# Optimization experiments

Hardware: AMD Instinct MI355X
Metric: run time of the kernel (lower is better)

The kernel has to match this reference:

```python
import jax, jax.numpy as jnp
import numpy as np

N = 6144      # nodes
IN = 512      # input_dim
D = 256       # HIDDEN_DIM (out_features per head)
H = 1         # HEADS
OUT = 128     # OUT_DIM
ALPHA = 0.2   # LeakyReLU slope
EPS = 1e-5    # LayerNorm eps


def _xavier(k, shape):
    fan_in, fan_out = shape[-2], shape[-1]
    lim = float(np.sqrt(6.0 / (fan_in + fan_out)))
    return jax.random.uniform(k, shape, jnp.float32, -lim, lim)


def _gat(x, W, a_src, a_dst, adj):
    # x: [N, IN], W: [IN, H*D], a_src/a_dst: [H, D], adj: [N, N] int
    n = x.shape[0]
    h = (x @ W).reshape(n, H, D)                       # [N, H, D]
    e1 = jnp.einsum('nhd,hd->nh', h, a_src)            # src score
    e2 = jnp.einsum('nhd,hd->nh', h, a_dst)            # dst score
    e = jax.nn.leaky_relu(e1[:, None, :] + e2[None, :, :], ALPHA)  # [N, N, H]
    e = jnp.where(adj[:, :, None] > 0, e, jnp.float32(-1e9))
    att = jnp.nan_to_num(jax.nn.softmax(e, axis=1), nan=0.0)       # softmax over dim -2 (j)
    out = jnp.einsum('nbh,bhd->nhd', att, h)           # weighted aggregation over j
    return out.reshape(n, H * D)                       # is_concat=True


def _ln(x, g, b):
    m = jnp.mean(x, axis=-1, keepdims=True)
    v = jnp.mean((x - m) ** 2, axis=-1, keepdims=True)
    return (x - m) * jax.lax.rsqrt(v + EPS) * g + b


def setup_inputs() -> dict:
    key = jax.random.key(0)
    ks = jax.random.split(key, 20)
    inp = {
        'x': jax.random.normal(ks[0], (N, IN), jnp.float32),
        'adj_cf': jax.random.randint(ks[1], (N, N), 0, 2, jnp.int32),
        'adj_org': jax.random.randint(ks[2], (N, N), 0, 2, jnp.int32),
        'adj_per': jax.random.randint(ks[3], (N, N), 0, 2, jnp.int32),
        'W_cf': _xavier(ks[4], (IN, H * D)),
        'a_src_cf': _xavier(ks[5], (H, D)),
        'a_dst_cf': _xavier(ks[6], (H, D)),
        'W_org': _xavier(ks[7], (IN, H * D)),
        'a_src_org': _xavier(ks[8], (H, D)),
        'a_dst_org': _xavier(ks[9], (H, D)),
        'W_per': _xavier(ks[10], (IN, H * D)),
        'a_src_per': _xavier(ks[11], (H, D)),
        'a_dst_per': _xavier(ks[12], (H, D)),
        'proj_W': _xavier(ks[13], (H * D, OUT)),
        'proj_b': jnp.zeros((OUT,), jnp.float32),
        'ln_g': jnp.ones((OUT,), jnp.float32),
        'ln_b': jnp.zeros((OUT,), jnp.float32),
        'alpha': jnp.ones((3, 1), jnp.float32),
    }
    return inp


def reference(x, adj_cf, adj_org, adj_per,
              W_cf, a_src_cf, a_dst_cf,
              W_org, a_src_org, a_dst_org,
              W_per, a_src_per, a_dst_per,
              proj_W, proj_b, ln_g, ln_b, alpha):
    # dropout layers are identity in eval mode
    h_cf = _gat(x, W_cf, a_src_cf, a_dst_cf, adj_cf)
    h_org = _gat(x, W_org, a_src_org, a_dst_org, adj_org)
    h_per = _gat(x, W_per, a_src_per, a_dst_per, adj_per)
    z_cf = _ln(h_cf @ proj_W + proj_b, ln_g, ln_b)
    z_org = _ln(h_org @ proj_W + proj_b, ln_g, ln_b)
    z_per = _ln(h_per @ proj_W + proj_b, ln_g, ln_b)
    w = jax.nn.softmax(alpha, axis=0)                  # [3, 1]
    z = w[0] * z_cf + w[1] * z_org + w[2] * z_per
    z = jnp.nan_to_num(z, nan=0.0, posinf=0.0, neginf=0.0)
    return (z, w)
```

## Files before the change

kernel.cpp:

```cpp
#include <hip/hip_runtime.h>

typedef _Float16 half_t;
typedef _Float16 f16x8 __attribute__((ext_vector_type(8)));
typedef _Float16 f16x4 __attribute__((ext_vector_type(4)));
typedef float f32x4 __attribute__((ext_vector_type(4)));
typedef unsigned long long u64;

#define NN 6144
#define IN_DIM 512
#define DD 256
#define OUT_DIM 128
#define SPLIT 3
#define JTILES 32
#define LOG2E 1.44269504088896340736f

__device__ __forceinline__ f32x4 mfma16(f16x8 a, f16x8 b, f32x4 c) {
  return __builtin_amdgcn_mfma_f32_16x16x32_f16(a, b, c, 0, 0, 0);
}

__global__ void cvt_x_kernel(const float* __restrict__ x, half_t* __restrict__ xh) {
  int idx = (blockIdx.x * 256 + threadIdx.x) * 4;
  float4 v = *(const float4*)(x + idx);
  f16x4 h;
  h[0] = (half_t)v.x; h[1] = (half_t)v.y; h[2] = (half_t)v.z; h[3] = (half_t)v.w;
  *(f16x4*)(xh + idx) = h;
}

__global__ void cvt_w_kernel(const float* __restrict__ W0, const float* __restrict__ W1,
                             const float* __restrict__ W2, const float* __restrict__ pW,
                             half_t* __restrict__ WT, half_t* __restrict__ pWT) {
  int y = blockIdx.y;
  int idx = blockIdx.x * 256 + threadIdx.x;
  if (y < 3) {
    const float* W = (y == 0) ? W0 : (y == 1) ? W1 : W2;
    int k = idx >> 8, n = idx & 255;
    WT[(size_t)y * DD * IN_DIM + (size_t)n * IN_DIM + k] = (half_t)W[idx];
  } else if (idx < DD * OUT_DIM) {
    int k = idx >> 7, o = idx & 127;
    pWT[(size_t)o * DD + k] = (half_t)pW[idx];
  }
}

__global__ __launch_bounds__(256, 2) void gemm1_kernel(
    const half_t* __restrict__ xh, const half_t* __restrict__ WT,
    const float* __restrict__ as0, const float* __restrict__ as1, const float* __restrict__ as2,
    const float* __restrict__ ad0, const float* __restrict__ ad1, const float* __restrict__ ad2,
    half_t* __restrict__ hT, float* __restrict__ e1, float* __restrict__ e2) {
  int v = blockIdx.y;
  int i0 = blockIdx.x * 64;
  int t = threadIdx.x;
  int lane = t & 63, w = t >> 6;
  int lr = lane & 15, lg = lane >> 4;
  const half_t* Wv = WT + (size_t)v * DD * IN_DIM;
  const float* asv = (v == 0) ? as0 : (v == 1) ? as1 : as2;
  const float* adv = (v == 0) ? ad0 : (v == 1) ? ad1 : ad2;
  f32x4 acc[4][4] = {};
  for (int kt = 0; kt < 16; ++kt) {
    int k = kt * 32 + lg * 8;
    f16x8 af[4], bf[4];
#pragma unroll
    for (int mf = 0; mf < 4; ++mf)
      af[mf] = *(const f16x8*)(xh + (size_t)(i0 + mf * 16 + lr) * IN_DIM + k);
#pragma unroll
    for (int nf = 0; nf < 4; ++nf)
      bf[nf] = *(const f16x8*)(Wv + (size_t)(w * 64 + nf * 16 + lr) * IN_DIM + k);
#pragma unroll
    for (int mf = 0; mf < 4; ++mf)
#pragma unroll
      for (int nf = 0; nf < 4; ++nf)
        acc[mf][nf] = mfma16(af[mf], bf[nf], acc[mf][nf]);
  }
  __shared__ half_t tr[4][64 * 64];
  __shared__ float ep1[4][64], ep2[4][64];
  char* trw = (char*)tr[w];
#pragma unroll
  for (int mf = 0; mf < 4; ++mf)
#pragma unroll
    for (int nf = 0; nf < 4; ++nf)
#pragma unroll
      for (int r = 0; r < 4; ++r) {
        int dl = nf * 16 + lr;
        int il = mf * 16 + lg * 4 + r;
        unsigned addr = (unsigned)((dl * 128 + il * 2) ^ ((dl & 7) << 4));
        *(half_t*)(trw + addr) = (half_t)acc[mf][nf][r];
      }
  float as_c[4], ad_c[4];
#pragma unroll
  for (int nf = 0; nf < 4; ++nf) {
    int col = w * 64 + nf * 16 + lr;
    as_c[nf] = asv[col];
    ad_c[nf] = adv[col];
  }
#pragma unroll
  for (int mf = 0; mf < 4; ++mf)
#pragma unroll
    for (int r = 0; r < 4; ++r) {
      float p1 = 0.f, p2 = 0.f;
#pragma unroll
      for (int nf = 0; nf < 4; ++nf) {
        p1 = fmaf(acc[mf][nf][r], as_c[nf], p1);
        p2 = fmaf(acc[mf][nf][r], ad_c[nf], p2);
      }
      p1 += __shfl_xor(p1, 1); p1 += __shfl_xor(p1, 2);
      p1 += __shfl_xor(p1, 4); p1 += __shfl_xor(p1, 8);
      p2 += __shfl_xor(p2, 1); p2 += __shfl_xor(p2, 2);
      p2 += __shfl_xor(p2, 4); p2 += __shfl_xor(p2, 8);
      if (lr == 0) {
        int il = mf * 16 + lg * 4 + r;
        ep1[w][il] = p1;
        ep2[w][il] = p2;
      }
    }
  __syncthreads();
  half_t* hTv = hT + (size_t)v * DD * NN;
#pragma unroll
  for (int c = 0; c < 8; ++c) {
    unsigned addr = (unsigned)((lane * 128 + c * 16) ^ ((lane & 7) << 4));
    f16x8 val = *(const f16x8*)(trw + addr);
    *(f16x8*)(hTv + (size_t)(w * 64 + lane) * NN + i0 + c * 8) = val;
  }
  if (t < 64) {
    e1[v * NN + i0 + t] = LOG2E * (ep1[0][t] + ep1[1][t] + ep1[2][t] + ep1[3][t]);
    e2[v * NN + i0 + t] = LOG2E * (ep2[0][t] + ep2[1][t] + ep2[2][t] + ep2[3][t]);
  }
}

__global__ void e2max_kernel(const float* __restrict__ e2, float* __restrict__ e2m) {
  int v = blockIdx.x;
  __shared__ float red[256];
  float m = -1e30f;
  for (int i = threadIdx.x; i < NN; i += 256) m = fmaxf(m, e2[v * NN + i]);
  red[threadIdx.x] = m;
  __syncthreads();
  for (int s = 128; s > 0; s >>= 1) {
    if (threadIdx.x < s) red[threadIdx.x] = fmaxf(red[threadIdx.x], red[threadIdx.x + s]);
    __syncthreads();
  }
  if (threadIdx.x == 0) e2m[v] = red[0];
}

__global__ __launch_bounds__(256, 2) void gat_kernel(
    const int* __restrict__ adj0, const int* __restrict__ adj1, const int* __restrict__ adj2,
    const half_t* __restrict__ hT,
    const float* __restrict__ e1g, const float* __restrict__ e2g,
    const float* __restrict__ e2maxg, half_t* __restrict__ pacc, float* __restrict__ pl) {
  int v = blockIdx.z, s = blockIdx.y;
  const int* __restrict__ adjv = (v == 0) ? adj0 : (v == 1) ? adj1 : adj2;
  int i0 = blockIdx.x * 64;
  int t = threadIdx.x;
  int lane = t & 63, w = t >> 6;
  int lr = lane & 15, lg = lane >> 4;
  int jq = t & 15, rg = t >> 4;
  __shared__ half_t hbuf[DD * 64];
  __shared__ half_t P0[64 * 64];
  __shared__ half_t P1[64 * 64];
  __shared__ float l_lds[64];
  const half_t* hTv = hT + (size_t)v * DD * NN;
  const float* e2v = e2g + v * NN;
  const int jt0 = s * JTILES;
  float e1r[4], mr[4];
  float e2mL = e2maxg[v];
#pragma unroll
  for (int it = 0; it < 4; ++it) {
    float e1i = e1g[v * NN + i0 + it * 16 + rg];
    e1r[it] = e1i;
    float sm = e1i + e2mL;
    mr[it] = fmaxf(sm, 0.2f * sm);
  }

  f32x4 acc[4][4] = {};
  float lpart[4] = {0.f, 0.f, 0.f, 0.f};
  int4 awA[4], awB[4];

  int sub = lane >> 3;
  int c_src = (lane & 7) ^ sub;
  auto gload = [&](int jt) {
    int j0 = jt * 64;
#pragma unroll
    for (int q = 0; q < 8; ++q) {
      int d = w * 64 + q * 8 + sub;
      const half_t* gp = hTv + (size_t)d * NN + j0 + c_src * 8;
      half_t* lp = hbuf + (w * 8 + q) * 512;
      __builtin_amdgcn_global_load_lds(
          (const __attribute__((address_space(1))) int*)gp,
          (__attribute__((address_space(3))) int*)lp, 16, 0, 0);
    }
  };
  auto load_adj = [&](int4 (&aw)[4], int jt) {
    int j0 = jt * 64;
#pragma unroll
    for (int it = 0; it < 4; ++it)
      aw[it] = *(const int4*)(adjv + (size_t)(i0 + it * 16 + rg) * NN + j0 + jq * 4);
  };
  auto comp_p = [&](const int4 (&aw)[4], int jt, char* pb) {
    int j0 = jt * 64;
    float4 e2q = *(const float4*)(e2v + j0 + jq * 4);
    float e2a[4] = {e2q.x, e2q.y, e2q.z, e2q.w};
#pragma unroll
    for (int it = 0; it < 4; ++it) {
      int il = it * 16 + rg;
      int a4[4] = {aw[it].x, aw[it].y, aw[it].z, aw[it].w};
      f16x4 ph;
      float ssum = 0.f;
#pragma unroll
      for (int c = 0; c < 4; ++c) {
        float s1 = e1r[it] + e2a[c];
        float u = fmaxf(s1, 0.2f * s1) - mr[it];
        float p = (a4[c] > 0) ? exp2f(u) : 0.f;
        ssum += p;
        ph[c] = (half_t)p;
      }
      lpart[it] += ssum;
      unsigned addr = (unsigned)((il * 128 + jq * 8) ^ ((il & 7) << 4));
      *(f16x4*)(pb + addr) = ph;
    }
  };
  auto do_mfma = [&](const char* pb) {
#pragma unroll
    for (int kf = 0; kf < 2; ++kf) {
      f16x8 bfr[4];
#pragma unroll
      for (int nf = 0; nf < 4; ++nf) {
        int d = w * 64 + nf * 16 + lr;
        unsigned ba = (unsigned)(d * 128 + ((kf * 64 + lg * 16) ^ ((lr & 7) << 4)));
        bfr[nf] = *(const f16x8*)((const char*)hbuf + ba);
      }
#pragma unroll
      for (int mf = 0; mf < 4; ++mf) {
        int row = mf * 16 + lr;
        unsigned pa = (unsigned)((row * 128 + kf * 64 + lg * 16) ^ ((row & 7) << 4));
        f16x8 af = *(const f16x8*)(pb + pa);
#pragma unroll
        for (int nf = 0; nf < 4; ++nf)
          acc[mf][nf] = mfma16(af, bfr[nf], acc[mf][nf]);
      }
    }
  };

  load_adj(awA, jt0);
  gload(jt0);
  load_adj(awB, jt0 + 1);
  comp_p(awA, jt0, (char*)P0);
  __syncthreads();

  for (int k = 0; k < JTILES; k += 2) {
    int jt = jt0 + k;
    do_mfma((char*)P0);
    __syncthreads();
    if (k + 1 < JTILES) {
      gload(jt + 1);
      comp_p(awB, jt + 1, (char*)P1);
    }
    if (k + 2 < JTILES) load_adj(awA, jt + 2);
    __syncthreads();
    if (k + 1 < JTILES) {
      do_mfma((char*)P1);
      __syncthreads();
      if (k + 2 < JTILES) {
        gload(jt + 2);
        comp_p(awA, jt + 2, (char*)P0);
      }
      if (k + 3 < JTILES) load_adj(awB, jt + 3);
      __syncthreads();
    }
  }

#pragma unroll
  for (int it = 0; it < 4; ++it) {
    float ssum = lpart[it];
    ssum += __shfl_xor(ssum, 1); ssum += __shfl_xor(ssum, 2);
    ssum += __shfl_xor(ssum, 4); ssum += __shfl_xor(ssum, 8);
    if (lr == 0) l_lds[it * 16 + rg] = ssum;
  }
  __syncthreads();
  size_t sl = (size_t)v * SPLIT + s;
  if (t < 64) pl[sl * NN + i0 + t] = l_lds[t];
  half_t* pa = pacc + sl * (size_t)NN * DD;
#pragma unroll
  for (int mf = 0; mf < 4; ++mf)
#pragma unroll
    for (int r = 0; r < 4; ++r) {
      int il = mf * 16 + lg * 4 + r;
#pragma unroll
      for (int nf = 0; nf < 4; ++nf)
        pa[(size_t)(i0 + il) * DD + w * 64 + nf * 16 + lr] = (half_t)acc[mf][nf][r];
    }
}

__global__ __launch_bounds__(64) void proj_kernel(
    const half_t* __restrict__ pacc, const float* __restrict__ pl,
    const half_t* __restrict__ pWT,
    const float* __restrict__ proj_b, const float* __restrict__ ln_g,
    const float* __restrict__ ln_b, const float* __restrict__ alpha,
    float* __restrict__ out) {
  int i0 = blockIdx.x * 16;
  int t = threadIdx.x;
  int lr = t & 15, lg = t >> 4;
  float a0 = alpha[0], a1 = alpha[1], a2 = alpha[2];
  float am = fmaxf(a0, fmaxf(a1, a2));
  float x0 = __expf(a0 - am), x1 = __expf(a1 - am), x2 = __expf(a2 - am);
  float inv = 1.f / (x0 + x1 + x2);
  float wv[3] = {x0 * inv, x1 * inv, x2 * inv};
  __shared__ float rlv[3][16];
  if (t < 48) {
    int v = t >> 4, i = t & 15;
    float l = pl[((size_t)v * SPLIT + 0) * NN + i0 + i] +
              pl[((size_t)v * SPLIT + 1) * NN + i0 + i] +
              pl[((size_t)v * SPLIT + 2) * NN + i0 + i];
    rlv[v][i] = (l > 0.f) ? 1.f / l : 0.f;
  }
  float pb[8], gg[8], bb[8];
#pragma unroll
  for (int nf = 0; nf < 8; ++nf) {
    pb[nf] = proj_b[nf * 16 + lr];
    gg[nf] = ln_g[nf * 16 + lr];
    bb[nf] = ln_b[nf * 16 + lr];
  }
  __syncthreads();
  f32x4 zacc[8] = {};
  for (int v = 0; v < 3; ++v) {
    float rl = rlv[v][lr];
    f32x4 yac[8] = {};
    const half_t* p0 = pacc + (((size_t)v * SPLIT + 0) * NN + i0 + lr) * DD;
    const half_t* p1 = pacc + (((size_t)v * SPLIT + 1) * NN + i0 + lr) * DD;
    const half_t* p2 = pacc + (((size_t)v * SPLIT + 2) * NN + i0 + lr) * DD;
    for (int kt = 0; kt < 8; ++kt) {
      int k = kt * 32 + lg * 8;
      f16x8 s0 = *(const f16x8*)(p0 + k);
      f16x8 s1 = *(const f16x8*)(p1 + k);
      f16x8 s2 = *(const f16x8*)(p2 + k);
      f16x8 af;
#pragma unroll
      for (int e = 0; e < 8; ++e)
        af[e] = (half_t)(((float)s0[e] + (float)s1[e] + (float)s2[e]) * rl);
#pragma unroll
      for (int nf = 0; nf < 8; ++nf) {
        f16x8 bf = *(const f16x8*)(pWT + (size_t)(nf * 16 + lr) * DD + k);
        yac[nf] = mfma16(af, bf, yac[nf]);
      }
    }
#pragma unroll
    for (int r = 0; r < 4; ++r) {
      float ssum = 0.f, q = 0.f;
#pragma unroll
      for (int nf = 0; nf < 8; ++nf) {
        float y = yac[nf][r] + pb[nf];
        yac[nf][r] = y;
        ssum += y; q += y * y;
      }
      ssum += __shfl_xor(ssum, 1); ssum += __shfl_xor(ssum, 2);
      ssum += __shfl_xor(ssum, 4); ssum += __shfl_xor(ssum, 8);
      q += __shfl_xor(q, 1); q += __shfl_xor(q, 2);
      q += __shfl_xor(q, 4); q += __shfl_xor(q, 8);
      float mean = ssum * (1.f / 128.f);
      float var = q * (1.f / 128.f) - mean * mean;
      float rstd = rsqrtf(var + 1e-5f);
      float wvv = wv[v];
#pragma unroll
      for (int nf = 0; nf < 8; ++nf)
        zacc[nf][r] += wvv * (yac[nf][r] - mean) * rstd;
    }
  }
#pragma unroll
  for (int nf = 0; nf < 8; ++nf)
#pragma unroll
    for (int r = 0; r < 4; ++r) {
      int row = i0 + lg * 4 + r;
      float z = zacc[nf][r] * gg[nf] + bb[nf];
      if (!isfinite(z)) z = 0.f;
      out[(size_t)row * OUT_DIM + nf * 16 + lr] = z;
    }
  if (blockIdx.x == 0 && t < 3) out[(size_t)NN * OUT_DIM + t] = wv[t];
}

extern "C" void kernel_launch(void* const* d_in, const int* in_sizes, int n_in,
                              void* d_out, int out_size, void* d_ws, size_t ws_size,
                              hipStream_t stream) {
  const float* x      = (const float*)d_in[0];
  const int*   adj_cf = (const int*)d_in[1];
  const int*   adj_or = (const int*)d_in[2];
  const int*   adj_pe = (const int*)d_in[3];
  const float* W_cf   = (const float*)d_in[4];
  const float* as_cf  = (const float*)d_in[5];
  const float* ad_cf  = (const float*)d_in[6];
  const float* W_or   = (const float*)d_in[7];
  const float* as_or  = (const float*)d_in[8];
  const float* ad_or  = (const float*)d_in[9];
  const float* W_pe   = (const float*)d_in[10];
  const float* as_pe  = (const float*)d_in[11];
  const float* ad_pe  = (const float*)d_in[12];
  const float* proj_W = (const float*)d_in[13];
  const float* proj_b = (const float*)d_in[14];
  const float* ln_g   = (const float*)d_in[15];
  const float* ln_b   = (const float*)d_in[16];
  const float* alpha  = (const float*)d_in[17];

  char* ws = (char*)d_ws;
  half_t* xh     = (half_t*)(ws + 0);
  half_t* WT     = (half_t*)(ws + 6291456);
  half_t* pWT    = (half_t*)(ws + 7077888);
  half_t* hT     = (half_t*)(ws + 7143424);
  float*  e1     = (float*)(ws + 16580608);
  float*  e2     = (float*)(ws + 16654336);
  float*  e2m    = (float*)(ws + 16728064);
  half_t* pacc   = (half_t*)(ws + 16728128);
  float*  pl     = (float*)(ws + 45039680);

  cvt_x_kernel<<<3072, 256, 0, stream>>>(x, xh);
  cvt_w_kernel<<<dim3(512, 4), 256, 0, stream>>>(W_cf, W_or, W_pe, proj_W, WT, pWT);
  gemm1_kernel<<<dim3(96, 3), 256, 0, stream>>>(xh, WT, as_cf, as_or, as_pe,
                                                ad_cf, ad_or, ad_pe, hT, e1, e2);
  e2max_kernel<<<3, 256, 0, stream>>>(e2, e2m);
  gat_kernel<<<dim3(96, SPLIT, 3), 256, 0, stream>>>(adj_cf, adj_or, adj_pe, hT,
                                                     e1, e2, e2m, pacc, pl);
  proj_kernel<<<384, 64, 0, stream>>>(pacc, pl, pWT, proj_b, ln_g, ln_b, alpha,
                                      (float*)d_out);
}
```

Before: 263.3 us.

## Double-buffer h tiles in GAT kernel and split j range four ways

```diff
diff --git a/kernel.cpp b/kernel.cpp
--- a/kernel.cpp
+++ b/kernel.cpp
@@ -10,8 +10,8 @@
 #define IN_DIM 512
 #define DD 256
 #define OUT_DIM 128
-#define SPLIT 3
-#define JTILES 32
+#define SPLIT 4
+#define JT 24
 #define LOG2E 1.44269504088896340736f
 
 __device__ __forceinline__ f32x4 mfma16(f16x8 a, f16x8 b, f32x4 c) {
@@ -151,13 +151,16 @@
   int lane = t & 63, w = t >> 6;
   int lr = lane & 15, lg = lane >> 4;
   int jq = t & 15, rg = t >> 4;
-  __shared__ half_t hbuf[DD * 64];
+
+  __shared__ half_t hbuf0[DD * 64];
+  __shared__ half_t hbuf1[DD * 64];
   __shared__ half_t P0[64 * 64];
   __shared__ half_t P1[64 * 64];
-  __shared__ float l_lds[64];
+
   const half_t* hTv = hT + (size_t)v * DD * NN;
   const float* e2v = e2g + v * NN;
-  const int jt0 = s * JTILES;
+  const int jbase = s * JT * 64;
+
   float e1r[4], mr[4];
   float e2mL = e2maxg[v];
 #pragma unroll
@@ -170,31 +173,27 @@
 
   f32x4 acc[4][4] = {};
   float lpart[4] = {0.f, 0.f, 0.f, 0.f};
-  int4 awA[4], awB[4];
 
   int sub = lane >> 3;
   int c_src = (lane & 7) ^ sub;
-  auto gload = [&](int jt) {
-    int j0 = jt * 64;
+  auto gload = [&](half_t* hb, int jt) {
+    int j0 = jbase + jt * 64;
 #pragma unroll
     for (int q = 0; q < 8; ++q) {
-      int d = w * 64 + q * 8 + sub;
-      const half_t* gp = hTv + (size_t)d * NN + j0 + c_src * 8;
-      half_t* lp = hbuf + (w * 8 + q) * 512;
+      const half_t* gp = hTv + (size_t)(w * 64 + q * 8 + sub) * NN + j0 + c_src * 8;
+      half_t* lp = hb + (w * 8 + q) * 512;
       __builtin_amdgcn_global_load_lds(
           (const __attribute__((address_space(1))) int*)gp,
           (__attribute__((address_space(3))) int*)lp, 16, 0, 0);
     }
   };
   auto load_adj = [&](int4 (&aw)[4], int jt) {
-    int j0 = jt * 64;
+    int j0 = jbase + jt * 64;
 #pragma unroll
     for (int it = 0; it < 4; ++it)
       aw[it] = *(const int4*)(adjv + (size_t)(i0 + it * 16 + rg) * NN + j0 + jq * 4);
   };
-  auto comp_p = [&](const int4 (&aw)[4], int jt, char* pb) {
-    int j0 = jt * 64;
-    float4 e2q = *(const float4*)(e2v + j0 + jq * 4);
+  auto comp_p = [&](const int4 (&aw)[4], const float4& e2q, char* pb) {
     float e2a[4] = {e2q.x, e2q.y, e2q.z, e2q.w};
 #pragma unroll
     for (int it = 0; it < 4; ++it) {
@@ -215,7 +214,7 @@
       *(f16x4*)(pb + addr) = ph;
     }
   };
-  auto do_mfma = [&](const char* pb) {
+  auto do_mfma = [&](const char* pb, const half_t* hb) {
 #pragma unroll
     for (int kf = 0; kf < 2; ++kf) {
       f16x8 bfr[4];
@@ -223,7 +222,7 @@
       for (int nf = 0; nf < 4; ++nf) {
         int d = w * 64 + nf * 16 + lr;
         unsigned ba = (unsigned)(d * 128 + ((kf * 64 + lg * 16) ^ ((lr & 7) << 4)));
-        bfr[nf] = *(const f16x8*)((const char*)hbuf + ba);
+        bfr[nf] = *(const f16x8*)((const char*)hb + ba);
       }
 #pragma unroll
       for (int mf = 0; mf < 4; ++mf) {
@@ -237,44 +236,43 @@
     }
   };
 
-  load_adj(awA, jt0);
-  gload(jt0);
-  load_adj(awB, jt0 + 1);
-  comp_p(awA, jt0, (char*)P0);
+  int4 awA[4], awB[4];
+  float4 e2A, e2B;
+
+  load_adj(awA, 0);
+  e2A = *(const float4*)(e2v + jbase + jq * 4);
+  gload(hbuf0, 0);
   __syncthreads();
 
-  for (int k = 0; k < JTILES; k += 2) {
-    int jt = jt0 + k;
-    do_mfma((char*)P0);
+  for (int tt = 0; tt < JT; tt += 2) {
+    comp_p(awA, e2A, (char*)P0);
     __syncthreads();
-    if (k + 1 < JTILES) {
-      gload(jt + 1);
-      comp_p(awB, jt + 1, (char*)P1);
-    }
-    if (k + 2 < JTILES) load_adj(awA, jt + 2);
+    {
+      load_adj(awB, tt + 1);
+      e2B = *(const float4*)(e2v + jbase + (tt + 1) * 64 + jq * 4);
+      gload(hbuf1, tt + 1);
+    }
+    do_mfma((char*)P0, hbuf0);
+
+    comp_p(awB, e2B, (char*)P1);
     __syncthreads();
-    if (k + 1 < JTILES) {
-      do_mfma((char*)P1);
-      __syncthreads();
-      if (k + 2 < JTILES) {
-        gload(jt + 2);
-        comp_p(awA, jt + 2, (char*)P0);
-      }
-      if (k + 3 < JTILES) load_adj(awB, jt + 3);
-      __syncthreads();
-    }
-  }
-
+    if (tt + 2 < JT) {
+      load_adj(awA, tt + 2);
+      e2A = *(const float4*)(e2v + jbase + (tt + 2) * 64 + jq * 4);
+      gload(hbuf0, tt + 2);
+    }
+    do_mfma((char*)P1, hbuf1);
+  }
+
+  size_t sl = (size_t)v * SPLIT + s;
 #pragma unroll
   for (int it = 0; it < 4; ++it) {
     float ssum = lpart[it];
     ssum += __shfl_xor(ssum, 1); ssum += __shfl_xor(ssum, 2);
     ssum += __shfl_xor(ssum, 4); ssum += __shfl_xor(ssum, 8);
-    if (lr == 0) l_lds[it * 16 + rg] = ssum;
-  }
-  __syncthreads();
-  size_t sl = (size_t)v * SPLIT + s;
-  if (t < 64) pl[sl * NN + i0 + t] = l_lds[t];
+    if (jq == 0) pl[sl * NN + i0 + it * 16 + rg] = ssum;
+  }
+
   half_t* pa = pacc + sl * (size_t)NN * DD;
 #pragma unroll
   for (int mf = 0; mf < 4; ++mf)
@@ -304,9 +302,10 @@
   __shared__ float rlv[3][16];
   if (t < 48) {
     int v = t >> 4, i = t & 15;
-    float l = pl[((size_t)v * SPLIT + 0) * NN + i0 + i] +
-              pl[((size_t)v * SPLIT + 1) * NN + i0 + i] +
-              pl[((size_t)v * SPLIT + 2) * NN + i0 + i];
+    float l = 0.f;
+#pragma unroll
+    for (int s = 0; s < SPLIT; ++s)
+      l += pl[((size_t)v * SPLIT + s) * NN + i0 + i];
     rlv[v][i] = (l > 0.f) ? 1.f / l : 0.f;
   }
   float pb[8], gg[8], bb[8];
@@ -324,15 +323,18 @@
     const half_t* p0 = pacc + (((size_t)v * SPLIT + 0) * NN + i0 + lr) * DD;
     const half_t* p1 = pacc + (((size_t)v * SPLIT + 1) * NN + i0 + lr) * DD;
     const half_t* p2 = pacc + (((size_t)v * SPLIT + 2) * NN + i0 + lr) * DD;
+    const half_t* p3 = pacc + (((size_t)v * SPLIT + 3) * NN + i0 + lr) * DD;
     for (int kt = 0; kt < 8; ++kt) {
       int k = kt * 32 + lg * 8;
       f16x8 s0 = *(const f16x8*)(p0 + k);
       f16x8 s1 = *(const f16x8*)(p1 + k);
       f16x8 s2 = *(const f16x8*)(p2 + k);
+      f16x8 s3 = *(const f16x8*)(p3 + k);
       f16x8 af;
 #pragma unroll
       for (int e = 0; e < 8; ++e)
-        af[e] = (half_t)(((float)s0[e] + (float)s1[e] + (float)s2[e]) * rl);
+        af[e] = (half_t)((((float)s0[e] + (float)s1[e]) +
+                          ((float)s2[e] + (float)s3[e])) * rl);
 #pragma unroll
       for (int nf = 0; nf < 8; ++nf) {
         f16x8 bf = *(const f16x8*)(pWT + (size_t)(nf * 16 + lr) * DD + k);
@@ -404,7 +406,7 @@
   float*  e2     = (float*)(ws + 16654336);
   float*  e2m    = (float*)(ws + 16728064);
   half_t* pacc   = (half_t*)(ws + 16728128);
-  float*  pl     = (float*)(ws + 45039680);
+  float*  pl     = (float*)(ws + 54476864);
 
   cvt_x_kernel<<<3072, 256, 0, stream>>>(x, xh);
   cvt_w_kernel<<<dim3(512, 4), 256, 0, stream>>>(W_cf, W_or, W_pe, proj_W, WT, pWT);
```

New measurement: 261.3 us. No clear change (-0.8%).
